# Performance work log

Measured on AMD Instinct MI355X. Metric: run time of the kernel, lower is better.

The kernel has to match this reference:

```python
import jax, jax.numpy as jnp
import numpy as np

N_NODES = 50000
N_EDGES = 800000
VOCAB = 1000
EMBED = 128
HIDDEN = 128
N_CLASSES = 10
N_GRAPHS = 64


def setup_inputs() -> dict:
    key = jax.random.key(0)
    ks = jax.random.split(key, 12)
    x_idx = jax.random.randint(ks[0], (N_NODES,), 0, VOCAB)
    edge_index = jax.random.randint(ks[1], (2, N_EDGES), 0, N_NODES)
    batch = jnp.sort(jax.random.randint(ks[2], (N_NODES,), 0, N_GRAPHS))
    s = lambda k, shp, fan: jax.random.normal(k, shp, jnp.float32) / jnp.sqrt(fan)
    return {
        "x_idx": x_idx,
        "edge_index": edge_index,
        "batch": batch,
        "embed_table": jax.random.normal(ks[3], (VOCAB, EMBED), jnp.float32),
        "Wl1": s(ks[4], (HIDDEN, EMBED), EMBED),
        "bl1": jnp.zeros((HIDDEN,), jnp.float32),
        "Wr1": s(ks[5], (HIDDEN, EMBED), EMBED),
        "Wl2": s(ks[6], (HIDDEN, HIDDEN), HIDDEN),
        "bl2": jnp.zeros((HIDDEN,), jnp.float32),
        "Wr2": s(ks[7], (HIDDEN, HIDDEN), HIDDEN),
        "linW": s(ks[8], (N_CLASSES, HIDDEN), HIDDEN),
        "linb": jnp.zeros((N_CLASSES,), jnp.float32),
    }


def _sage_conv(x, src, dst, Wl, bl, Wr):
    # mean aggregation of source features into destination nodes (PyG SAGEConv, aggr='mean')
    msg_sum = jax.ops.segment_sum(x[src], dst, num_segments=N_NODES)  # [N, d]
    cnt = jax.ops.segment_sum(jnp.ones((src.shape[0],), x.dtype), dst, num_segments=N_NODES)
    agg = msg_sum / jnp.maximum(cnt, 1.0)[:, None]
    # out = lin_l(agg) + lin_r(x); lin_l has bias, lin_r has none
    return agg @ Wl.T + bl + x @ Wr.T


def reference(x_idx, edge_index, batch, embed_table, Wl1, bl1, Wr1, Wl2, bl2, Wr2, linW, linb):
    src, dst = edge_index[0], edge_index[1]
    x = embed_table[x_idx]  # [N, EMBED]
    x = jax.nn.relu(_sage_conv(x, src, dst, Wl1, bl1, Wr1))
    x = jax.nn.relu(_sage_conv(x, src, dst, Wl2, bl2, Wr2))
    # global mean pool over graphs
    g_sum = jax.ops.segment_sum(x, batch, num_segments=N_GRAPHS)  # [G, HIDDEN]
    g_cnt = jax.ops.segment_sum(jnp.ones((x.shape[0],), x.dtype), batch, num_segments=N_GRAPHS)
    pooled = g_sum / jnp.maximum(g_cnt, 1.0)[:, None]
    return pooled @ linW.T + linb  # [G, N_CLASSES]
```

## Files before the change

### kernel.cpp

```cpp
#include <hip/hip_runtime.h>

#define N_NODES 50000
#define N_EDGES 800000
#define N_GRAPHS 64
#define SCAN_BLOCKS 196

#define NCHUNK 32
#define CHUNK_E (N_EDGES / NCHUNK)
#define NRANGE 4
#define RSZ (N_NODES / NRANGE)

#define K1_HIST (NCHUNK * NRANGE)
#define K1_EMBED (N_NODES * 16 / 256)
#define K1_PREP 32

typedef __bf16 bf16x8 __attribute__((ext_vector_type(8)));
typedef float f32x4 __attribute__((ext_vector_type(4)));

static __device__ __forceinline__ unsigned short f2bf(float f) {
    union { float f; unsigned u; } v; v.f = f;
    unsigned u = v.u;
    u += 0x7fffu + ((u >> 16) & 1u);
    return (unsigned short)(u >> 16);
}
static __device__ __forceinline__ float bflo(unsigned w) {
    union { unsigned u; float f; } v; v.u = w << 16; return v.f;
}
static __device__ __forceinline__ float bfhi(unsigned w) {
    union { unsigned u; float f; } v; v.u = w & 0xffff0000u; return v.f;
}

__global__ __launch_bounds__(256) void k1_kernel(const int* __restrict__ dst,
                                                 int* __restrict__ part,
                                                 const int* __restrict__ x_idx,
                                                 const float* __restrict__ table,
                                                 unsigned short* __restrict__ X,
                                                 const float* __restrict__ Wl1,
                                                 const float* __restrict__ Wr1,
                                                 const float* __restrict__ Wl2,
                                                 const float* __restrict__ Wr2,
                                                 unsigned short* __restrict__ blob,
                                                 float* __restrict__ gsum) {
    const int b = blockIdx.x;
    if (b < K1_HIST) {
        __shared__ int h[RSZ];
        const int c = b >> 2;
        const int r = b & 3;
        const int rbase = r * RSZ;
        for (int i = threadIdx.x; i < RSZ; i += 256) h[i] = 0;
        __syncthreads();
        const int4* d4 = (const int4*)(dst + c * CHUNK_E);
        for (int i = threadIdx.x; i < CHUNK_E / 4; i += 256) {
            int4 d = d4[i];
            unsigned a;
            a = (unsigned)(d.x - rbase); if (a < RSZ) atomicAdd(&h[a], 1);
            a = (unsigned)(d.y - rbase); if (a < RSZ) atomicAdd(&h[a], 1);
            a = (unsigned)(d.z - rbase); if (a < RSZ) atomicAdd(&h[a], 1);
            a = (unsigned)(d.w - rbase); if (a < RSZ) atomicAdd(&h[a], 1);
        }
        __syncthreads();
        int* p = part + (size_t)c * N_NODES + rbase;
        for (int i = threadIdx.x; i < RSZ; i += 256) p[i] = h[i];
    } else if (b < K1_HIST + K1_EMBED) {
        int i = (b - K1_HIST) * 256 + threadIdx.x;
        int n = i >> 4, cq = i & 15;
        const float4* src = (const float4*)(table + (size_t)x_idx[n] * 128 + cq * 8);
        float4 a = src[0], bb = src[1];
        uint4 o;
        o.x = (unsigned)f2bf(a.x)  | ((unsigned)f2bf(a.y)  << 16);
        o.y = (unsigned)f2bf(a.z)  | ((unsigned)f2bf(a.w)  << 16);
        o.z = (unsigned)f2bf(bb.x) | ((unsigned)f2bf(bb.y) << 16);
        o.w = (unsigned)f2bf(bb.z) | ((unsigned)f2bf(bb.w) << 16);
        ((uint4*)X)[i] = o;
    } else {
        int s = (b - K1_HIST - K1_EMBED) * 256 + threadIdx.x;
        gsum[s] = 0.f;
        int g = s >> 12;
        int sl = s & 4095;
        int fidx = sl >> 6, lane = sl & 63;
        int m = fidx >> 5, kk = (fidx >> 3) & 3, tile = fidx & 7;
        const float* W = g ? (m ? Wr2 : Wl2) : (m ? Wr1 : Wl1);
        int n  = tile * 16 + (lane & 15);
        int k0 = kk * 32 + (lane >> 4) * 8;
        const float4* src = (const float4*)(W + n * 128 + k0);
        float4 a = src[0], bb = src[1];
        uint4 o;
        o.x = (unsigned)f2bf(a.x)  | ((unsigned)f2bf(a.y)  << 16);
        o.y = (unsigned)f2bf(a.z)  | ((unsigned)f2bf(a.w)  << 16);
        o.z = (unsigned)f2bf(bb.x) | ((unsigned)f2bf(bb.y) << 16);
        o.w = (unsigned)f2bf(bb.z) | ((unsigned)f2bf(bb.w) << 16);
        ((uint4*)blob)[s] = o;
    }
}

__global__ __launch_bounds__(256) void cntsum_kernel(const int* __restrict__ part,
                                                     int* __restrict__ cnt,
                                                     int* __restrict__ bsum) {
    int t = threadIdx.x;
    int n = blockIdx.x * 256 + t;
    int s = 0;
    if (n < N_NODES) {
#pragma unroll
        for (int c = 0; c < NCHUNK; ++c) s += part[(size_t)c * N_NODES + n];
        cnt[n] = s;
    }
#pragma unroll
    for (int off = 32; off > 0; off >>= 1) s += __shfl_down(s, off, 64);
    __shared__ int ws[4];
    if ((t & 63) == 0) ws[t >> 6] = s;
    __syncthreads();
    if (t == 0) bsum[blockIdx.x] = ws[0] + ws[1] + ws[2] + ws[3];
}

__global__ __launch_bounds__(256) void rowptroff_kernel(const int* __restrict__ cnt,
                                                        const int* __restrict__ bsum,
                                                        const int* __restrict__ part,
                                                        int* __restrict__ rowptr,
                                                        int* __restrict__ off) {
    __shared__ int sb[256];
    __shared__ int sd[256];
    int t = threadIdx.x;
    sb[t] = (t < SCAN_BLOCKS) ? bsum[t] : 0;
    __syncthreads();
    for (int o = 1; o < 256; o <<= 1) {
        int add = (t >= o) ? sb[t - o] : 0;
        __syncthreads();
        sb[t] += add;
        __syncthreads();
    }
    int boff = (blockIdx.x > 0) ? sb[blockIdx.x - 1] : 0;

    int i = blockIdx.x * 256 + t;
    int v = (i < N_NODES) ? cnt[i] : 0;
    sd[t] = v;
    __syncthreads();
    for (int o = 1; o < 256; o <<= 1) {
        int add = (t >= o) ? sd[t - o] : 0;
        __syncthreads();
        sd[t] += add;
        __syncthreads();
    }
    int excl = sd[t] - v + boff;
    if (i < N_NODES) {
        rowptr[i] = excl;
        if (i == N_NODES - 1) rowptr[N_NODES] = excl + v;
        int run = excl;
#pragma unroll
        for (int c = 0; c < NCHUNK; ++c) {
            off[(size_t)c * N_NODES + i] = run;
            run += part[(size_t)c * N_NODES + i];
        }
    }
}

__global__ __launch_bounds__(256) void scatter_kernel(const int* __restrict__ src,
                                                      const int* __restrict__ dst,
                                                      const int* __restrict__ off,
                                                      int* __restrict__ csr) {
    __shared__ int h[RSZ];
    const int c = blockIdx.x >> 2;
    const int r = blockIdx.x & 3;
    const int rbase = r * RSZ;
    const int* o = off + (size_t)c * N_NODES + rbase;
    for (int i = threadIdx.x; i < RSZ; i += 256) h[i] = o[i];
    __syncthreads();
    const int4* d4 = (const int4*)(dst + c * CHUNK_E);
    const int4* s4 = (const int4*)(src + c * CHUNK_E);
    for (int i = threadIdx.x; i < CHUNK_E / 4; i += 256) {
        int4 d = d4[i];
        int4 s = s4[i];
        unsigned a;
        a = (unsigned)(d.x - rbase); if (a < RSZ) csr[atomicAdd(&h[a], 1)] = s.x;
        a = (unsigned)(d.y - rbase); if (a < RSZ) csr[atomicAdd(&h[a], 1)] = s.y;
        a = (unsigned)(d.z - rbase); if (a < RSZ) csr[atomicAdd(&h[a], 1)] = s.z;
        a = (unsigned)(d.w - rbase); if (a < RSZ) csr[atomicAdd(&h[a], 1)] = s.w;
    }
}

__global__ __launch_bounds__(256) void agg_kernel(const unsigned short* __restrict__ X,
                                                  const int* __restrict__ rowptr,
                                                  const int* __restrict__ csr,
                                                  unsigned short* __restrict__ AGG) {
    const int t = threadIdx.x;
    const int lane = t & 63;
    const int f = lane & 15;
    const int n = blockIdx.x * 16 + (t >> 6) * 4 + (lane >> 4);
    int beg = rowptr[n], end = rowptr[n + 1];
    const char* Xb = (const char*)X + f * 16;
    float a0 = 0.f, a1 = 0.f, a2 = 0.f, a3 = 0.f,
          a4 = 0.f, a5 = 0.f, a6 = 0.f, a7 = 0.f;
    int i = beg;
    for (; i + 4 <= end; i += 4) {
        int s0 = csr[i], s1 = csr[i + 1], s2 = csr[i + 2], s3 = csr[i + 3];
        uint4 v0 = *(const uint4*)(Xb + (size_t)s0 * 256);
        uint4 v1 = *(const uint4*)(Xb + (size_t)s1 * 256);
        uint4 v2 = *(const uint4*)(Xb + (size_t)s2 * 256);
        uint4 v3 = *(const uint4*)(Xb + (size_t)s3 * 256);
        a0 += (bflo(v0.x) + bflo(v1.x)) + (bflo(v2.x) + bflo(v3.x));
        a1 += (bfhi(v0.x) + bfhi(v1.x)) + (bfhi(v2.x) + bfhi(v3.x));
        a2 += (bflo(v0.y) + bflo(v1.y)) + (bflo(v2.y) + bflo(v3.y));
        a3 += (bfhi(v0.y) + bfhi(v1.y)) + (bfhi(v2.y) + bfhi(v3.y));
        a4 += (bflo(v0.z) + bflo(v1.z)) + (bflo(v2.z) + bflo(v3.z));
        a5 += (bfhi(v0.z) + bfhi(v1.z)) + (bfhi(v2.z) + bfhi(v3.z));
        a6 += (bflo(v0.w) + bflo(v1.w)) + (bflo(v2.w) + bflo(v3.w));
        a7 += (bfhi(v0.w) + bfhi(v1.w)) + (bfhi(v2.w) + bfhi(v3.w));
    }
    for (; i < end; ++i) {
        uint4 v0 = *(const uint4*)(Xb + (size_t)csr[i] * 256);
        a0 += bflo(v0.x); a1 += bfhi(v0.x);
        a2 += bflo(v0.y); a3 += bfhi(v0.y);
        a4 += bflo(v0.z); a5 += bfhi(v0.z);
        a6 += bflo(v0.w); a7 += bfhi(v0.w);
    }
    float inv = 1.f / (float)max(end - beg, 1);
    uint4 o;
    o.x = (unsigned)f2bf(a0 * inv) | ((unsigned)f2bf(a1 * inv) << 16);
    o.y = (unsigned)f2bf(a2 * inv) | ((unsigned)f2bf(a3 * inv) << 16);
    o.z = (unsigned)f2bf(a4 * inv) | ((unsigned)f2bf(a5 * inv) << 16);
    o.w = (unsigned)f2bf(a6 * inv) | ((unsigned)f2bf(a7 * inv) << 16);
    *(uint4*)((char*)AGG + (size_t)n * 256 + f * 16) = o;
}

__global__ __launch_bounds__(256) void gemm_kernel(const unsigned short* __restrict__ A0,
                                                   const unsigned short* __restrict__ A1,
                                                   const unsigned short* __restrict__ wblob,
                                                   const float* __restrict__ bias,
                                                   unsigned short* __restrict__ Y) {
    __shared__ char lds[65536];
    const int t = threadIdx.x, lane = t & 63, w = t >> 6;
    const int row0 = blockIdx.x * 128 + w * 32;

    {
        const char* src = (const char*)wblob + w * 16384 + lane * 16;
        char* dst = lds + w * 16384;
#pragma unroll
        for (int i = 0; i < 16; ++i) {
            __builtin_amdgcn_global_load_lds(
                (const __attribute__((address_space(1))) unsigned*)(src + i * 1024),
                (__attribute__((address_space(3))) unsigned*)(dst + i * 1024), 16, 0, 0);
        }
    }
    __syncthreads();

    f32x4 acc[2][8];
#pragma unroll
    for (int rt = 0; rt < 2; ++rt)
#pragma unroll
        for (int tl = 0; tl < 8; ++tl) acc[rt][tl] = (f32x4){0.f, 0.f, 0.f, 0.f};

    int rA = min(row0 + (lane & 15),      N_NODES - 1);
    int rB = min(row0 + 16 + (lane & 15), N_NODES - 1);
    const int kl = (lane >> 4) * 8;

#pragma unroll
    for (int km = 0; km < 8; ++km) {
        const unsigned short* A = (km < 4) ? A0 : A1;
        int k0 = (km & 3) * 32 + kl;
        bf16x8 a0 = *(const bf16x8*)(A + (size_t)rA * 128 + k0);
        bf16x8 a1 = *(const bf16x8*)(A + (size_t)rB * 128 + k0);
        const char* bbase = lds + km * 8192 + lane * 16;
#pragma unroll
        for (int tile = 0; tile < 8; ++tile) {
            bf16x8 b = *(const bf16x8*)(bbase + tile * 1024);
            acc[0][tile] = __builtin_amdgcn_mfma_f32_16x16x32_bf16(a0, b, acc[0][tile], 0, 0, 0);
            acc[1][tile] = __builtin_amdgcn_mfma_f32_16x16x32_bf16(a1, b, acc[1][tile], 0, 0, 0);
        }
    }

    const int c     = lane & 15;
    const int rbase = (lane >> 4) * 4;
#pragma unroll
    for (int rt = 0; rt < 2; ++rt) {
#pragma unroll
        for (int tile = 0; tile < 8; ++tile) {
            int col = tile * 16 + c;
            float bv = bias[col];
#pragma unroll
            for (int j = 0; j < 4; ++j) {
                int r = row0 + rt * 16 + rbase + j;
                if (r < N_NODES)
                    Y[(size_t)r * 128 + col] = f2bf(fmaxf(acc[rt][tile][j] + bv, 0.f));
            }
        }
    }
}

__global__ __launch_bounds__(256) void gemm_pool_kernel(const unsigned short* __restrict__ A0,
                                                        const unsigned short* __restrict__ A1,
                                                        const unsigned short* __restrict__ wblob,
                                                        const float* __restrict__ bias,
                                                        const int* __restrict__ batch,
                                                        float* __restrict__ gsum) {
    __shared__ char lds[65536];
    const int t = threadIdx.x, lane = t & 63, w = t >> 6;
    const int brow0 = blockIdx.x * 128;
    const int row0  = brow0 + w * 32;

    {
        const char* src = (const char*)wblob + w * 16384 + lane * 16;
        char* dst = lds + w * 16384;
#pragma unroll
        for (int i = 0; i < 16; ++i) {
            __builtin_amdgcn_global_load_lds(
                (const __attribute__((address_space(1))) unsigned*)(src + i * 1024),
                (__attribute__((address_space(3))) unsigned*)(dst + i * 1024), 16, 0, 0);
        }
    }
    __syncthreads();

    f32x4 acc[2][8];
#pragma unroll
    for (int rt = 0; rt < 2; ++rt)
#pragma unroll
        for (int tl = 0; tl < 8; ++tl) acc[rt][tl] = (f32x4){0.f, 0.f, 0.f, 0.f};

    int rA = min(row0 + (lane & 15),      N_NODES - 1);
    int rB = min(row0 + 16 + (lane & 15), N_NODES - 1);
    const int kl = (lane >> 4) * 8;

#pragma unroll
    for (int km = 0; km < 8; ++km) {
        const unsigned short* A = (km < 4) ? A0 : A1;
        int k0 = (km & 3) * 32 + kl;
        bf16x8 a0 = *(const bf16x8*)(A + (size_t)rA * 128 + k0);
        bf16x8 a1 = *(const bf16x8*)(A + (size_t)rB * 128 + k0);
        const char* bbase = lds + km * 8192 + lane * 16;
#pragma unroll
        for (int tile = 0; tile < 8; ++tile) {
            bf16x8 b = *(const bf16x8*)(bbase + tile * 1024);
            acc[0][tile] = __builtin_amdgcn_mfma_f32_16x16x32_bf16(a0, b, acc[0][tile], 0, 0, 0);
            acc[1][tile] = __builtin_amdgcn_mfma_f32_16x16x32_bf16(a1, b, acc[1][tile], 0, 0, 0);
        }
    }

    __syncthreads();
    float* ftile = (float*)lds;
    const int c     = lane & 15;
    const int rbase = (lane >> 4) * 4;
#pragma unroll
    for (int rt = 0; rt < 2; ++rt) {
#pragma unroll
        for (int tile = 0; tile < 8; ++tile) {
            int col = tile * 16 + c;
            float bv = bias[col];
#pragma unroll
            for (int j = 0; j < 4; ++j) {
                int lr = w * 32 + rt * 16 + rbase + j;
                ftile[lr * 128 + col] = fmaxf(acc[rt][tile][j] + bv, 0.f);
            }
        }
    }
    __syncthreads();

    const int col  = t & 127;
    const int half = t >> 7;
    float s = 0.f;
    int curg = -1;
    for (int rr = 0; rr < 64; ++rr) {
        int r = brow0 + half * 64 + rr;
        if (r >= N_NODES) break;
        int g = batch[r];
        if (g != curg) {
            if (curg >= 0) atomicAdd(&gsum[curg * 128 + col], s);
            curg = g; s = 0.f;
        }
        s += ftile[(half * 64 + rr) * 128 + col];
    }
    if (curg >= 0) atomicAdd(&gsum[curg * 128 + col], s);
}

__global__ void final_kernel(const float* __restrict__ gsum, const int* __restrict__ batch,
                             const float* __restrict__ linW, const float* __restrict__ linb,
                             float* __restrict__ out) {
    int t = blockIdx.x * 256 + threadIdx.x;
    if (t >= N_GRAPHS * 10) return;
    int g = t / 10, j = t % 10;
    int bnd[2];
    for (int c = 0; c < 2; ++c) {
        int target = g + c;
        int lo = 0, hi = N_NODES;
        while (lo < hi) { int mid = (lo + hi) >> 1; if (batch[mid] < target) lo = mid + 1; else hi = mid; }
        bnd[c] = lo;
    }
    float invc = 1.f / (float)max(bnd[1] - bnd[0], 1);
    float s = 0.f;
    for (int k = 0; k < 128; ++k) s += gsum[g * 128 + k] * linW[j * 128 + k];
    out[t] = linb[j] + s * invc;
}

extern "C" void kernel_launch(void* const* d_in, const int* in_sizes, int n_in,
                              void* d_out, int out_size, void* d_ws, size_t ws_size,
                              hipStream_t stream) {
    const int*   x_idx = (const int*)d_in[0];
    const int*   eidx  = (const int*)d_in[1];
    const int*   batch = (const int*)d_in[2];
    const float* table = (const float*)d_in[3];
    const float* Wl1   = (const float*)d_in[4];
    const float* bl1   = (const float*)d_in[5];
    const float* Wr1   = (const float*)d_in[6];
    const float* Wl2   = (const float*)d_in[7];
    const float* bl2   = (const float*)d_in[8];
    const float* Wr2   = (const float*)d_in[9];
    const float* linW  = (const float*)d_in[10];
    const float* linb  = (const float*)d_in[11];
    float*       out   = (float*)d_out;

    const int* src = eidx;
    const int* dst = eidx + N_EDGES;

    unsigned short* X    = (unsigned short*)d_ws;
    unsigned short* AGG  = X   + (size_t)N_NODES * 128;
    unsigned short* Y1   = AGG + (size_t)N_NODES * 128;
    unsigned short* blob = Y1  + (size_t)N_NODES * 128;
    float* gsum = (float*)(blob + 65536);
    int* cnt    = (int*)(gsum + N_GRAPHS * 128);
    int* rowptr = cnt + N_NODES;
    int* csr    = rowptr + (N_NODES + 1);
    int* bsum   = csr + N_EDGES;
    int* part   = bsum + SCAN_BLOCKS;
    int* off    = part + (size_t)NCHUNK * N_NODES;

    k1_kernel<<<K1_HIST + K1_EMBED + K1_PREP, 256, 0, stream>>>(
        dst, part, x_idx, table, X, Wl1, Wr1, Wl2, Wr2, blob, gsum);
    cntsum_kernel   <<<SCAN_BLOCKS, 256, 0, stream>>>(part, cnt, bsum);
    rowptroff_kernel<<<SCAN_BLOCKS, 256, 0, stream>>>(cnt, bsum, part, rowptr, off);
    scatter_kernel  <<<NCHUNK * NRANGE, 256, 0, stream>>>(src, dst, off, csr);

    agg_kernel <<<dim3(N_NODES / 16), 256, 0, stream>>>(X, rowptr, csr, AGG);
    gemm_kernel<<<dim3((N_NODES + 127) / 128), 256, 0, stream>>>(AGG, X, blob, bl1, Y1);
    agg_kernel      <<<dim3(N_NODES / 16), 256, 0, stream>>>(Y1, rowptr, csr, AGG);
    gemm_pool_kernel<<<dim3((N_NODES + 127) / 128), 256, 0, stream>>>(AGG, Y1, blob + 32768, bl2, batch, gsum);

    final_kernel<<<3, 256, 0, stream>>>(gsum, batch, linW, linb, out);
}
```

Before: 153.5 us.

## Shrink CSR partial-count buffers to bytes, rebalance chunks, and widen aggregation gather

Cuts edge chunks from 32 to 8 and raises node ranges from 4 to 8. Stores the per-chunk histogram as unsigned bytes, which reduces the partial-count and offset traffic in the scan kernels. Unrolls the aggregation gather to eight neighbors with nontemporal loads to expose more memory-level parallelism. Risks: histogram and scatter blocks now each scan four times more edges with half as many blocks; byte counts silently wrap if a node gets more than 255 edges in one chunk; nontemporal hints may reduce cache reuse of the gathered feature rows.

```diff
diff --git a/kernel.cpp b/kernel.cpp
--- a/kernel.cpp
+++ b/kernel.cpp
@@ -5,9 +5,9 @@
 #define N_GRAPHS 64
 #define SCAN_BLOCKS 196
 
-#define NCHUNK 32
+#define NCHUNK 8
 #define CHUNK_E (N_EDGES / NCHUNK)
-#define NRANGE 4
+#define NRANGE 8
 #define RSZ (N_NODES / NRANGE)
 
 #define K1_HIST (NCHUNK * NRANGE)
@@ -16,6 +16,7 @@
 
 typedef __bf16 bf16x8 __attribute__((ext_vector_type(8)));
 typedef float f32x4 __attribute__((ext_vector_type(4)));
+typedef unsigned u32x4 __attribute__((ext_vector_type(4)));
 
 static __device__ __forceinline__ unsigned short f2bf(float f) {
     union { float f; unsigned u; } v; v.f = f;
@@ -30,8 +31,23 @@
     union { unsigned u; float f; } v; v.u = w & 0xffff0000u; return v.f;
 }
 
+#define ACC8(A, v) do { \
+    A[0] += bflo((v)[0]); A[1] += bfhi((v)[0]); \
+    A[2] += bflo((v)[1]); A[3] += bfhi((v)[1]); \
+    A[4] += bflo((v)[2]); A[5] += bfhi((v)[2]); \
+    A[6] += bflo((v)[3]); A[7] += bfhi((v)[3]); } while (0)
+
+static __device__ __forceinline__ uint4 cvt2x4(float4 a, float4 b) {
+    uint4 o;
+    o.x = (unsigned)f2bf(a.x) | ((unsigned)f2bf(a.y) << 16);
+    o.y = (unsigned)f2bf(a.z) | ((unsigned)f2bf(a.w) << 16);
+    o.z = (unsigned)f2bf(b.x) | ((unsigned)f2bf(b.y) << 16);
+    o.w = (unsigned)f2bf(b.z) | ((unsigned)f2bf(b.w) << 16);
+    return o;
+}
+
 __global__ __launch_bounds__(256) void k1_kernel(const int* __restrict__ dst,
-                                                 int* __restrict__ part,
+                                                 unsigned char* __restrict__ part,
                                                  const int* __restrict__ x_idx,
                                                  const float* __restrict__ table,
                                                  unsigned short* __restrict__ X,
@@ -44,8 +60,8 @@
     const int b = blockIdx.x;
     if (b < K1_HIST) {
         __shared__ int h[RSZ];
-        const int c = b >> 2;
-        const int r = b & 3;
+        const int c = b >> 3;
+        const int r = b & 7;
         const int rbase = r * RSZ;
         for (int i = threadIdx.x; i < RSZ; i += 256) h[i] = 0;
         __syncthreads();
@@ -59,19 +75,13 @@
             a = (unsigned)(d.w - rbase); if (a < RSZ) atomicAdd(&h[a], 1);
         }
         __syncthreads();
-        int* p = part + (size_t)c * N_NODES + rbase;
-        for (int i = threadIdx.x; i < RSZ; i += 256) p[i] = h[i];
+        unsigned char* p = part + (size_t)c * N_NODES + rbase;
+        for (int i = threadIdx.x; i < RSZ; i += 256) p[i] = (unsigned char)h[i];
     } else if (b < K1_HIST + K1_EMBED) {
         int i = (b - K1_HIST) * 256 + threadIdx.x;
         int n = i >> 4, cq = i & 15;
         const float4* src = (const float4*)(table + (size_t)x_idx[n] * 128 + cq * 8);
-        float4 a = src[0], bb = src[1];
-        uint4 o;
-        o.x = (unsigned)f2bf(a.x)  | ((unsigned)f2bf(a.y)  << 16);
-        o.y = (unsigned)f2bf(a.z)  | ((unsigned)f2bf(a.w)  << 16);
-        o.z = (unsigned)f2bf(bb.x) | ((unsigned)f2bf(bb.y) << 16);
-        o.w = (unsigned)f2bf(bb.z) | ((unsigned)f2bf(bb.w) << 16);
-        ((uint4*)X)[i] = o;
+        ((uint4*)X)[i] = cvt2x4(src[0], src[1]);
     } else {
         int s = (b - K1_HIST - K1_EMBED) * 256 + threadIdx.x;
         gsum[s] = 0.f;
@@ -83,17 +93,11 @@
         int n  = tile * 16 + (lane & 15);
         int k0 = kk * 32 + (lane >> 4) * 8;
         const float4* src = (const float4*)(W + n * 128 + k0);
-        float4 a = src[0], bb = src[1];
-        uint4 o;
-        o.x = (unsigned)f2bf(a.x)  | ((unsigned)f2bf(a.y)  << 16);
-        o.y = (unsigned)f2bf(a.z)  | ((unsigned)f2bf(a.w)  << 16);
-        o.z = (unsigned)f2bf(bb.x) | ((unsigned)f2bf(bb.y) << 16);
-        o.w = (unsigned)f2bf(bb.z) | ((unsigned)f2bf(bb.w) << 16);
-        ((uint4*)blob)[s] = o;
-    }
-}
-
-__global__ __launch_bounds__(256) void cntsum_kernel(const int* __restrict__ part,
+        ((uint4*)blob)[s] = cvt2x4(src[0], src[1]);
+    }
+}
+
+__global__ __launch_bounds__(256) void cntsum_kernel(const unsigned char* __restrict__ part,
                                                      int* __restrict__ cnt,
                                                      int* __restrict__ bsum) {
     int t = threadIdx.x;
@@ -114,7 +118,7 @@
 
 __global__ __launch_bounds__(256) void rowptroff_kernel(const int* __restrict__ cnt,
                                                         const int* __restrict__ bsum,
-                                                        const int* __restrict__ part,
+                                                        const unsigned char* __restrict__ part,
                                                         int* __restrict__ rowptr,
                                                         int* __restrict__ off) {
     __shared__ int sb[256];
@@ -158,8 +162,8 @@
                                                       const int* __restrict__ off,
                                                       int* __restrict__ csr) {
     __shared__ int h[RSZ];
-    const int c = blockIdx.x >> 2;
-    const int r = blockIdx.x & 3;
+    const int c = blockIdx.x >> 3;
+    const int r = blockIdx.x & 7;
     const int rbase = r * RSZ;
     const int* o = off + (size_t)c * N_NODES + rbase;
     for (int i = threadIdx.x; i < RSZ; i += 256) h[i] = o[i];
@@ -187,37 +191,40 @@
     const int n = blockIdx.x * 16 + (t >> 6) * 4 + (lane >> 4);
     int beg = rowptr[n], end = rowptr[n + 1];
     const char* Xb = (const char*)X + f * 16;
-    float a0 = 0.f, a1 = 0.f, a2 = 0.f, a3 = 0.f,
-          a4 = 0.f, a5 = 0.f, a6 = 0.f, a7 = 0.f;
+    float a[8];
+#pragma unroll
+    for (int k = 0; k < 8; ++k) a[k] = 0.f;
     int i = beg;
-    for (; i + 4 <= end; i += 4) {
-        int s0 = csr[i], s1 = csr[i + 1], s2 = csr[i + 2], s3 = csr[i + 3];
-        uint4 v0 = *(const uint4*)(Xb + (size_t)s0 * 256);
-        uint4 v1 = *(const uint4*)(Xb + (size_t)s1 * 256);
-        uint4 v2 = *(const uint4*)(Xb + (size_t)s2 * 256);
-        uint4 v3 = *(const uint4*)(Xb + (size_t)s3 * 256);
-        a0 += (bflo(v0.x) + bflo(v1.x)) + (bflo(v2.x) + bflo(v3.x));
-        a1 += (bfhi(v0.x) + bfhi(v1.x)) + (bfhi(v2.x) + bfhi(v3.x));
-        a2 += (bflo(v0.y) + bflo(v1.y)) + (bflo(v2.y) + bflo(v3.y));
-        a3 += (bfhi(v0.y) + bfhi(v1.y)) + (bfhi(v2.y) + bfhi(v3.y));
-        a4 += (bflo(v0.z) + bflo(v1.z)) + (bflo(v2.z) + bflo(v3.z));
-        a5 += (bfhi(v0.z) + bfhi(v1.z)) + (bfhi(v2.z) + bfhi(v3.z));
-        a6 += (bflo(v0.w) + bflo(v1.w)) + (bflo(v2.w) + bflo(v3.w));
-        a7 += (bfhi(v0.w) + bfhi(v1.w)) + (bfhi(v2.w) + bfhi(v3.w));
-    }
-    for (; i < end; ++i) {
-        uint4 v0 = *(const uint4*)(Xb + (size_t)csr[i] * 256);
-        a0 += bflo(v0.x); a1 += bfhi(v0.x);
-        a2 += bflo(v0.y); a3 += bfhi(v0.y);
-        a4 += bflo(v0.z); a5 += bfhi(v0.z);
-        a6 += bflo(v0.w); a7 += bfhi(v0.w);
+    for (; i + 8 <= end; i += 8) {
+        int s0 = csr[i + 0], s1 = csr[i + 1], s2 = csr[i + 2], s3 = csr[i + 3];
+        int s4 = csr[i + 4], s5 = csr[i + 5], s6 = csr[i + 6], s7 = csr[i + 7];
+        u32x4 v0 = __builtin_nontemporal_load((const u32x4*)(Xb + (size_t)s0 * 256));
+        u32x4 v1 = __builtin_nontemporal_load((const u32x4*)(Xb + (size_t)s1 * 256));
+        u32x4 v2 = __builtin_nontemporal_load((const u32x4*)(Xb + (size_t)s2 * 256));
+        u32x4 v3 = __builtin_nontemporal_load((const u32x4*)(Xb + (size_t)s3 * 256));
+        u32x4 v4 = __builtin_nontemporal_load((const u32x4*)(Xb + (size_t)s4 * 256));
+        u32x4 v5 = __builtin_nontemporal_load((const u32x4*)(Xb + (size_t)s5 * 256));
+        u32x4 v6 = __builtin_nontemporal_load((const u32x4*)(Xb + (size_t)s6 * 256));
+        u32x4 v7 = __builtin_nontemporal_load((const u32x4*)(Xb + (size_t)s7 * 256));
+        ACC8(a, v0); ACC8(a, v1); ACC8(a, v2); ACC8(a, v3);
+        ACC8(a, v4); ACC8(a, v5); ACC8(a, v6); ACC8(a, v7);
+    }
+    for (; i + 2 <= end; i += 2) {
+        int s0 = csr[i], s1 = csr[i + 1];
+        u32x4 v0 = __builtin_nontemporal_load((const u32x4*)(Xb + (size_t)s0 * 256));
+        u32x4 v1 = __builtin_nontemporal_load((const u32x4*)(Xb + (size_t)s1 * 256));
+        ACC8(a, v0); ACC8(a, v1);
+    }
+    if (i < end) {
+        u32x4 v0 = __builtin_nontemporal_load((const u32x4*)(Xb + (size_t)csr[i] * 256));
+        ACC8(a, v0);
     }
     float inv = 1.f / (float)max(end - beg, 1);
     uint4 o;
-    o.x = (unsigned)f2bf(a0 * inv) | ((unsigned)f2bf(a1 * inv) << 16);
-    o.y = (unsigned)f2bf(a2 * inv) | ((unsigned)f2bf(a3 * inv) << 16);
-    o.z = (unsigned)f2bf(a4 * inv) | ((unsigned)f2bf(a5 * inv) << 16);
-    o.w = (unsigned)f2bf(a6 * inv) | ((unsigned)f2bf(a7 * inv) << 16);
+    o.x = (unsigned)f2bf(a[0] * inv) | ((unsigned)f2bf(a[1] * inv) << 16);
+    o.y = (unsigned)f2bf(a[2] * inv) | ((unsigned)f2bf(a[3] * inv) << 16);
+    o.z = (unsigned)f2bf(a[4] * inv) | ((unsigned)f2bf(a[5] * inv) << 16);
+    o.w = (unsigned)f2bf(a[6] * inv) | ((unsigned)f2bf(a[7] * inv) << 16);
     *(uint4*)((char*)AGG + (size_t)n * 256 + f * 16) = o;
 }
 
@@ -417,8 +424,8 @@
     int* rowptr = cnt + N_NODES;
     int* csr    = rowptr + (N_NODES + 1);
     int* bsum   = csr + N_EDGES;
-    int* part   = bsum + SCAN_BLOCKS;
-    int* off    = part + (size_t)NCHUNK * N_NODES;
+    int* off    = bsum + SCAN_BLOCKS;
+    unsigned char* part = (unsigned char*)(off + (size_t)NCHUNK * N_NODES);
 
     k1_kernel<<<K1_HIST + K1_EMBED + K1_PREP, 256, 0, stream>>>(
         dst, part, x_idx, table, X, Wl1, Wr1, Wl2, Wr2, blob, gsum);
```

Measured after the change: 261.5 us. +70.4%, slower.
